# Kernel tuning notes

Measured on AMD Instinct MI355X. Metric: run time of the kernel, lower is better.

Reference implementation:

```python
import jax, jax.numpy as jnp
import numpy as np

V, D, H, L, DFF = 32000, 512, 8, 6, 2048
B, T = 64, 256
PAD_IDX = 1


def _pos_encoding(t, d):
    pos = jnp.arange(t, dtype=jnp.float32)[:, None]          # [t,1]
    i2 = jnp.arange(0, d, 2, dtype=jnp.float32)              # [d/2]
    ang = pos / jnp.power(10000.0, i2 / d)                   # [t,d/2]
    pe = jnp.zeros((t, d), dtype=jnp.float32)
    pe = pe.at[:, 0::2].set(jnp.sin(ang))
    pe = pe.at[:, 1::2].set(jnp.cos(ang))
    return pe


def _ln(x, g, b):
    mu = x.mean(-1, keepdims=True)
    var = ((x - mu) ** 2).mean(-1, keepdims=True)
    return (x - mu) * jax.lax.rsqrt(var + 1e-5) * g + b


def _mha(xq, xkv, Wq, Wk, Wv, Wo, bo, causal):
    b, tq, d = xq.shape
    tk = xkv.shape[1]
    hd = d // H
    q = (xq @ Wq).reshape(b, tq, H, hd)
    k = (xkv @ Wk).reshape(b, tk, H, hd)
    v = (xkv @ Wv).reshape(b, tk, H, hd)
    wei = jnp.einsum('bqhd,bkhd->bhqk', q, k) * (hd ** -0.5)
    if causal:
        mask = jnp.tril(jnp.ones((tq, tk), dtype=bool))
        wei = jnp.where(mask, wei, -jnp.inf)
    wei = jax.nn.softmax(wei, axis=-1)
    out = jnp.einsum('bhqk,bkhd->bqhd', wei, v).reshape(b, tq, d)
    return out @ Wo + bo


def _ffn(x, W1, b1, W2, b2):
    return jax.nn.relu(x @ W1 + b1) @ W2 + b2


def setup_inputs() -> dict:
    key = jax.random.key(0)
    ks = iter(jax.random.split(key, 64))
    nrm = lambda shape: (jax.random.normal(next(ks), shape, dtype=jnp.float32) * 0.02)
    inp = {
        'idx': jax.random.randint(next(ks), (B, T), 0, V),
        'idx_enc': jax.random.randint(next(ks), (B, T), 0, V),
        'targets': jax.random.randint(next(ks), (B, T), 0, V),
        'emb_dec': nrm((V, D)),
        'emb_enc': nrm((V, D)),
        # encoder stacks [L, ...]
        'enc_Wq': nrm((L, D, D)), 'enc_Wk': nrm((L, D, D)), 'enc_Wv': nrm((L, D, D)),
        'enc_Wo': nrm((L, D, D)), 'enc_bo': jnp.zeros((L, D)),
        'enc_ln_g': jnp.ones((L, 2, D)), 'enc_ln_b': jnp.zeros((L, 2, D)),
        'enc_W1': nrm((L, D, DFF)), 'enc_b1': jnp.zeros((L, DFF)),
        'enc_W2': nrm((L, DFF, D)), 'enc_b2': jnp.zeros((L, D)),
        # decoder stacks [L, ...]
        'dec_Wq_sa': nrm((L, D, D)), 'dec_Wk_sa': nrm((L, D, D)), 'dec_Wv_sa': nrm((L, D, D)),
        'dec_Wo_sa': nrm((L, D, D)), 'dec_bo_sa': jnp.zeros((L, D)),
        'dec_Wq_xa': nrm((L, D, D)), 'dec_Wk_xa': nrm((L, D, D)), 'dec_Wv_xa': nrm((L, D, D)),
        'dec_Wo_xa': nrm((L, D, D)), 'dec_bo_xa': jnp.zeros((L, D)),
        'dec_ln_g': jnp.ones((L, 4, D)), 'dec_ln_b': jnp.zeros((L, 4, D)),
        'dec_W1': nrm((L, D, DFF)), 'dec_b1': jnp.zeros((L, DFF)),
        'dec_W2': nrm((L, DFF, D)), 'dec_b2': jnp.zeros((L, D)),
        'lnf_g': jnp.ones((D,)), 'lnf_b': jnp.zeros((D,)),
        'Wlm': nrm((D, V)), 'blm': jnp.zeros((V,)),
    }
    return inp


def reference(idx, idx_enc, targets, emb_dec, emb_enc,
              enc_Wq, enc_Wk, enc_Wv, enc_Wo, enc_bo, enc_ln_g, enc_ln_b,
              enc_W1, enc_b1, enc_W2, enc_b2,
              dec_Wq_sa, dec_Wk_sa, dec_Wv_sa, dec_Wo_sa, dec_bo_sa,
              dec_Wq_xa, dec_Wk_xa, dec_Wv_xa, dec_Wo_xa, dec_bo_xa,
              dec_ln_g, dec_ln_b, dec_W1, dec_b1, dec_W2, dec_b2,
              lnf_g, lnf_b, Wlm, blm):
    t_dec = idx.shape[1]
    t_enc = idx_enc.shape[1]
    pe = _pos_encoding(256, D)
    # encoder
    y = emb_enc[idx_enc] + pe[:t_enc]
    for l in range(L):
        h = _ln(y, enc_ln_g[l, 0], enc_ln_b[l, 0])
        y = y + _mha(h, h, enc_Wq[l], enc_Wk[l], enc_Wv[l], enc_Wo[l], enc_bo[l], causal=False)
        h = _ln(y, enc_ln_g[l, 1], enc_ln_b[l, 1])
        y = y + _ffn(h, enc_W1[l], enc_b1[l], enc_W2[l], enc_b2[l])
    # decoder
    x = emb_dec[idx] + pe[:t_dec]
    for l in range(L):
        h = _ln(x, dec_ln_g[l, 0], dec_ln_b[l, 0])
        x = x + _mha(h, h, dec_Wq_sa[l], dec_Wk_sa[l], dec_Wv_sa[l], dec_Wo_sa[l], dec_bo_sa[l], causal=True)
        hq = _ln(x, dec_ln_g[l, 1], dec_ln_b[l, 1])
        hk = _ln(y, dec_ln_g[l, 2], dec_ln_b[l, 2])
        x = x + _mha(hq, hk, dec_Wq_xa[l], dec_Wk_xa[l], dec_Wv_xa[l], dec_Wo_xa[l], dec_bo_xa[l], causal=False)
        h = _ln(x, dec_ln_g[l, 3], dec_ln_b[l, 3])
        x = x + _ffn(h, dec_W1[l], dec_b1[l], dec_W2[l], dec_b2[l])
    x = _ln(x, lnf_g, lnf_b)
    logits = (x @ Wlm + blm).reshape(-1, V)  # [B*T, V]
    # cross entropy with ignore_index = PAD_IDX, mean over non-ignored
    tgt = targets.reshape(-1)
    logp = jax.nn.log_softmax(logits, axis=-1)
    nll = -jnp.take_along_axis(logp, tgt[:, None], axis=-1)[:, 0]
    valid = (tgt != PAD_IDX).astype(logits.dtype)
    loss = jnp.sum(nll * valid) / jnp.maximum(jnp.sum(valid), 1.0)
    return logits, loss
```

## Files before the change

kernel.cpp:

```cpp
#include <hip/hip_runtime.h>

typedef __attribute__((ext_vector_type(8))) short s8v;
typedef __attribute__((ext_vector_type(4))) float f4v;
using u16 = unsigned short;

__device__ __forceinline__ u16 f2bf(float f) {
  union { float f; unsigned u; } v; v.f = f;
  return (u16)((v.u + 0x7FFFu + ((v.u >> 16) & 1u)) >> 16);
}

__global__ __launch_bounds__(256) void pe_kernel(float* __restrict__ pe) {
  int i = blockIdx.x * 256 + threadIdx.x;
  int t = i >> 8, p = i & 255;
  float ex = (2.f * (float)p) / 512.f;
  float ang = (float)t * expf(-ex * 9.210340371976184f);
  pe[t * 512 + 2 * p]     = sinf(ang);
  pe[t * 512 + 2 * p + 1] = cosf(ang);
}

__global__ __launch_bounds__(256) void wconv_kernel(const float* __restrict__ in,
    u16* __restrict__ out, int R, int C, size_t dstride) {
  __shared__ float tile[64][65];
  const size_t mat = (size_t)R * C;
  const float* src = in + (size_t)blockIdx.z * mat;
  u16* dst = out + (size_t)blockIdx.z * dstride;
  int r0 = blockIdx.x * 64, c0 = blockIdx.y * 64;
  int tr = threadIdx.x >> 6, tc = threadIdx.x & 63;
#pragma unroll
  for (int i = 0; i < 16; ++i)
    tile[i * 4 + tr][tc] = src[(size_t)(r0 + i * 4 + tr) * C + (c0 + tc)];
  __syncthreads();
#pragma unroll
  for (int i = 0; i < 16; ++i)
    dst[(size_t)(c0 + i * 4 + tr) * R + (r0 + tc)] = f2bf(tile[tc][i * 4 + tr]);
}

__global__ __launch_bounds__(256) void embed_kernel(const int* __restrict__ idx,
    const float* __restrict__ emb, const float* __restrict__ pe, float* __restrict__ y) {
  int i = blockIdx.x * 256 + threadIdx.x;
  int row = i >> 7, c = (i & 127) * 4;
  int t = row & 255;
  int tok = idx[row];
  f4v e = *(const f4v*)(emb + (size_t)tok * 512 + c);
  f4v p = *(const f4v*)(pe + (size_t)t * 512 + c);
  *(f4v*)(y + (size_t)row * 512 + c) = e + p;
}

__global__ __launch_bounds__(256) void ln_kernel(const float* __restrict__ x,
    const float* __restrict__ g, const float* __restrict__ b, u16* __restrict__ out) {
  int row = blockIdx.x * 4 + (threadIdx.x >> 6);
  int lane = threadIdx.x & 63;
  const float* xr = x + (size_t)row * 512 + lane * 8;
  f4v v0 = *(const f4v*)xr;
  f4v v1 = *(const f4v*)(xr + 4);
  float s = v0[0] + v0[1] + v0[2] + v0[3] + v1[0] + v1[1] + v1[2] + v1[3];
#pragma unroll
  for (int o = 1; o < 64; o <<= 1) s += __shfl_xor(s, o);
  float mu = s * (1.f / 512.f);
  float q = 0.f;
#pragma unroll
  for (int j = 0; j < 4; ++j) {
    float d0 = v0[j] - mu; q += d0 * d0;
    float d1 = v1[j] - mu; q += d1 * d1;
  }
#pragma unroll
  for (int o = 1; o < 64; o <<= 1) q += __shfl_xor(q, o);
  float rs = rsqrtf(q * (1.f / 512.f) + 1e-5f);
  f4v g0 = *(const f4v*)(g + lane * 8), g1 = *(const f4v*)(g + lane * 8 + 4);
  f4v b0 = *(const f4v*)(b + lane * 8), b1 = *(const f4v*)(b + lane * 8 + 4);
  s8v ov;
#pragma unroll
  for (int j = 0; j < 4; ++j) {
    ov[j]     = (short)f2bf((v0[j] - mu) * rs * g0[j] + b0[j]);
    ov[4 + j] = (short)f2bf((v1[j] - mu) * rs * g1[j] + b1[j]);
  }
  *(s8v*)(out + (size_t)row * 512 + lane * 8) = ov;
}

template<int WR, int MW, int NW, int HAS_BIAS, int ADD_RES, int RELU,
         int OUT_BF16, int WLOSS, int NT>
__global__ __launch_bounds__(MW * NW * 64, 2) void gemm_mfma(
    const u16* __restrict__ A, const u16* __restrict__ Bt,
    const float* __restrict__ bias, const float* __restrict__ res,
    void* __restrict__ outp, int M, int N, int K,
    float* __restrict__ pmax, float* __restrict__ psum) {
  constexpr int BM = MW * WR * 16;
  constexpr int BN = NW * 64;
  constexpr int THREADS = MW * NW * 64;
  constexpr int STEP = THREADS / 8;
  __shared__ __align__(16) u16 As[2][BM * 64];
  __shared__ __align__(16) u16 Bs[2][BN * 64];
  const int tid = threadIdx.x, lane = tid & 63, w = tid >> 6;
  int nx = gridDim.x;
  int flat = blockIdx.y * nx + blockIdx.x;
  int per = (nx * gridDim.y) >> 3;
  int sw = (flat & 7) * per + (flat >> 3);
  int by = sw / nx, bx = sw - by * nx;
  const int m0 = bx * BM, n0 = by * BN;
  const int wm = (w / NW) * (WR * 16), wn = (w % NW) * 64;
  const int lhi = lane >> 4, llo = lane & 15;
  const int srow = tid >> 3;
  const int sl = tid & 7;
  const int gcol = (sl ^ (srow & 7)) * 8;

  const u16* Ag = A + (size_t)(m0 + srow) * K + gcol;
  const u16* Bg = Bt + (size_t)(n0 + srow) * K + gcol;
  const size_t rstep = (size_t)STEP * K;

  auto STAGE = [&](int b, int kt) {
#pragma unroll
    for (int q = 0; q < BM / STEP; ++q)
      __builtin_amdgcn_global_load_lds(
          (const __attribute__((address_space(1))) void*)(Ag + q * rstep + kt),
          (__attribute__((address_space(3))) void*)(&As[b][(q * STEP + srow) * 64 + sl * 8]),
          16, 0, 0);
#pragma unroll
    for (int q = 0; q < BN / STEP; ++q)
      __builtin_amdgcn_global_load_lds(
          (const __attribute__((address_space(1))) void*)(Bg + q * rstep + kt),
          (__attribute__((address_space(3))) void*)(&Bs[b][(q * STEP + srow) * 64 + sl * 8]),
          16, 0, 0);
  };
  const int sx = llo & 7;

  f4v acc[WR][4] = {};
  const int nk = K >> 6;
  STAGE(0, 0);
  asm volatile("s_waitcnt vmcnt(0)" ::: "memory");
  __builtin_amdgcn_s_barrier();
  __builtin_amdgcn_sched_barrier(0);
  int cur = 0;
  for (int t = 0; t < nk; ++t) {
    if (t + 1 < nk) STAGE(cur ^ 1, (t + 1) * 64);
#pragma unroll
    for (int kk = 0; kk < 2; ++kk) {
      s8v af[WR], bfv[4];
#pragma unroll
      for (int i = 0; i < WR; ++i)
        af[i] = *(const s8v*)&As[cur][(wm + i * 16 + llo) * 64 + (((kk * 4 + lhi) ^ sx) * 8)];
#pragma unroll
      for (int j = 0; j < 4; ++j)
        bfv[j] = *(const s8v*)&Bs[cur][(wn + j * 16 + llo) * 64 + (((kk * 4 + lhi) ^ sx) * 8)];
      __builtin_amdgcn_s_setprio(1);
#pragma unroll
      for (int i = 0; i < WR; ++i)
#pragma unroll
        for (int j = 0; j < 4; ++j)
          acc[i][j] = __builtin_amdgcn_mfma_f32_16x16x32_bf16(af[i], bfv[j], acc[i][j], 0, 0, 0);
      __builtin_amdgcn_s_setprio(0);
    }
    asm volatile("s_waitcnt vmcnt(0)" ::: "memory");
    __builtin_amdgcn_s_barrier();
    __builtin_amdgcn_sched_barrier(0);
    cur ^= 1;
  }

  if (OUT_BF16) {
    float bvj[4];
#pragma unroll
    for (int j = 0; j < 4; ++j)
      bvj[j] = HAS_BIAS ? bias[n0 + wn + j * 16 + llo] : 0.f;
#pragma unroll
    for (int i = 0; i < WR; ++i) {
#pragma unroll
      for (int j = 0; j < 4; ++j) {
        int col = n0 + wn + j * 16 + llo;
#pragma unroll
        for (int r = 0; r < 4; ++r) {
          int row = m0 + wm + i * 16 + lhi * 4 + r;
          float v = acc[i][j][r] + bvj[j];
          if (RELU) v = fmaxf(v, 0.f);
          ((u16*)outp)[(size_t)row * N + col] = f2bf(v);
        }
      }
    }
  } else {
    float* lb = (float*)&As[0][0];
    float* wbuf = lb + w * 1088;
    f4v bias4 = {0.f, 0.f, 0.f, 0.f};
    if (HAS_BIAS) bias4 = *(const f4v*)(bias + n0 + wn + llo * 4);
    float* lbm = lb + 9216;
    float* lbs = lb + 10240;
#pragma unroll
    for (int i = 0; i < WR; ++i) {
#pragma unroll
      for (int j = 0; j < 4; ++j)
#pragma unroll
        for (int r = 0; r < 4; ++r)
          wbuf[(lhi * 4 + r) * 68 + j * 16 + llo] = acc[i][j][r];
      asm volatile("s_waitcnt lgkmcnt(0)" ::: "memory");
      __builtin_amdgcn_sched_barrier(0);
#pragma unroll
      for (int p = 0; p < 4; ++p) {
        int r16 = p * 4 + lhi;
        f4v v4 = *(const f4v*)&wbuf[r16 * 68 + llo * 4];
        v4 += bias4;
        int grow = m0 + wm + i * 16 + r16;
        int gcol4 = n0 + wn + llo * 4;
        if (ADD_RES) v4 += *(const f4v*)(res + (size_t)grow * N + gcol4);
        if (RELU) {
          v4[0] = fmaxf(v4[0], 0.f); v4[1] = fmaxf(v4[1], 0.f);
          v4[2] = fmaxf(v4[2], 0.f); v4[3] = fmaxf(v4[3], 0.f);
        }
        float* dst = (float*)outp + (size_t)grow * N + gcol4;
        if (NT) __builtin_nontemporal_store(v4, (f4v*)dst);
        else    *(f4v*)dst = v4;
        if (WLOSS) {
          float mx = fmaxf(fmaxf(v4[0], v4[1]), fmaxf(v4[2], v4[3]));
          mx = fmaxf(mx, __shfl_xor(mx, 1));
          mx = fmaxf(mx, __shfl_xor(mx, 2));
          mx = fmaxf(mx, __shfl_xor(mx, 4));
          mx = fmaxf(mx, __shfl_xor(mx, 8));
          float sum = __expf(v4[0] - mx) + __expf(v4[1] - mx)
                    + __expf(v4[2] - mx) + __expf(v4[3] - mx);
          sum += __shfl_xor(sum, 1); sum += __shfl_xor(sum, 2);
          sum += __shfl_xor(sum, 4); sum += __shfl_xor(sum, 8);
          if (llo == 0) {
            int lr = wm + i * 16 + r16;
            lbm[lr * 4 + (wn >> 6)] = mx;
            lbs[lr * 4 + (wn >> 6)] = sum;
          }
        }
      }
      asm volatile("s_waitcnt lgkmcnt(0)" ::: "memory");
      __builtin_amdgcn_sched_barrier(0);
    }
    if (WLOSS) {
      __syncthreads();
      if (tid < 256) {
        float m = lbm[tid * 4];
        m = fmaxf(fmaxf(m, lbm[tid * 4 + 1]), fmaxf(lbm[tid * 4 + 2], lbm[tid * 4 + 3]));
        float ss = lbs[tid * 4 + 0] * __expf(lbm[tid * 4 + 0] - m)
                 + lbs[tid * 4 + 1] * __expf(lbm[tid * 4 + 1] - m)
                 + lbs[tid * 4 + 2] * __expf(lbm[tid * 4 + 2] - m)
                 + lbs[tid * 4 + 3] * __expf(lbm[tid * 4 + 3] - m);
        int ntile = N >> 8;
        pmax[(size_t)(m0 + tid) * ntile + by] = m;
        psum[(size_t)(m0 + tid) * ntile + by] = ss;
      }
    }
  }
}

__global__ __launch_bounds__(256) void attn_kernel(
    const u16* __restrict__ Qp, int qs, const u16* __restrict__ Kp,
    const u16* __restrict__ Vp, int kvs, u16* __restrict__ Ob, int causal) {
  __shared__ __align__(16) u16 Ks[256][72];
  __shared__ __align__(16) u16 Vt[64][264];
  __shared__ __align__(16) u16 Ps[4][16][264];
  const int tid = threadIdx.x, lane = tid & 63, w = tid >> 6;
  const int b = blockIdx.x >> 3, h = blockIdx.x & 7;
  const size_t qbase  = (size_t)b * 256 * qs  + (size_t)h * 64;
  const size_t kvbase = (size_t)b * 256 * kvs + (size_t)h * 64;
  const size_t obase  = (size_t)b * 256 * 512 + (size_t)h * 64;
  {
    int t0 = tid >> 3, d0 = (tid & 7) * 8;
#pragma unroll
    for (int it = 0; it < 8; ++it) {
      int t = it * 32 + t0;
      s8v kv = *(const s8v*)(Kp + kvbase + (size_t)t * kvs + d0);
      *(s8v*)&Ks[t][d0] = kv;
      s8v vv = *(const s8v*)(Vp + kvbase + (size_t)t * kvs + d0);
#pragma unroll
      for (int j = 0; j < 8; ++j) Vt[d0 + j][t] = (u16)vv[j];
    }
  }
  __syncthreads();
  const int lhi = lane >> 4, llo = lane & 15;
  for (int qc = 0; qc < 4; ++qc) {
    const int qr0 = w * 64 + qc * 16;
    s8v aq0 = *(const s8v*)(Qp + qbase + (size_t)(qr0 + llo) * qs + lhi * 8);
    s8v aq1 = *(const s8v*)(Qp + qbase + (size_t)(qr0 + llo) * qs + 32 + lhi * 8);
    f4v S[16];
#pragma unroll
    for (int c = 0; c < 16; ++c) {
      s8v bk0 = *(const s8v*)&Ks[c * 16 + llo][lhi * 8];
      s8v bk1 = *(const s8v*)&Ks[c * 16 + llo][32 + lhi * 8];
      f4v z = {0.f, 0.f, 0.f, 0.f};
      z = __builtin_amdgcn_mfma_f32_16x16x32_bf16(aq0, bk0, z, 0, 0, 0);
      S[c] = __builtin_amdgcn_mfma_f32_16x16x32_bf16(aq1, bk1, z, 0, 0, 0);
    }
#pragma unroll
    for (int r = 0; r < 4; ++r) {
      const int tq = qr0 + lhi * 4 + r;
      float mx = -1e30f;
#pragma unroll
      for (int c = 0; c < 16; ++c) {
        float s = S[c][r] * 0.125f;
        if (causal && (c * 16 + llo) > tq) s = -1e30f;
        S[c][r] = s;
        mx = fmaxf(mx, s);
      }
      mx = fmaxf(mx, __shfl_xor(mx, 1));
      mx = fmaxf(mx, __shfl_xor(mx, 2));
      mx = fmaxf(mx, __shfl_xor(mx, 4));
      mx = fmaxf(mx, __shfl_xor(mx, 8));
      float sum = 0.f;
#pragma unroll
      for (int c = 0; c < 16; ++c) { float p = __expf(S[c][r] - mx); S[c][r] = p; sum += p; }
      sum += __shfl_xor(sum, 1); sum += __shfl_xor(sum, 2);
      sum += __shfl_xor(sum, 4); sum += __shfl_xor(sum, 8);
      float inv = 1.f / sum;
#pragma unroll
      for (int c = 0; c < 16; ++c)
        Ps[w][lhi * 4 + r][c * 16 + llo] = f2bf(S[c][r] * inv);
    }
    asm volatile("s_waitcnt lgkmcnt(0)" ::: "memory");
    f4v o[4] = {};
#pragma unroll
    for (int kb = 0; kb < 8; ++kb) {
      s8v pa = *(const s8v*)&Ps[w][llo][kb * 32 + lhi * 8];
#pragma unroll
      for (int nb = 0; nb < 4; ++nb) {
        s8v bv = *(const s8v*)&Vt[nb * 16 + llo][kb * 32 + lhi * 8];
        o[nb] = __builtin_amdgcn_mfma_f32_16x16x32_bf16(pa, bv, o[nb], 0, 0, 0);
      }
    }
#pragma unroll
    for (int nb = 0; nb < 4; ++nb)
#pragma unroll
      for (int r = 0; r < 4; ++r)
        Ob[obase + (size_t)(qr0 + lhi * 4 + r) * 512 + nb * 16 + llo] = f2bf(o[nb][r]);
  }
}

__global__ __launch_bounds__(256) void loss_lse_kernel(const float* __restrict__ pmax,
    const float* __restrict__ psum, const float* __restrict__ logits,
    const int* __restrict__ tgt, float* __restrict__ nll, float* __restrict__ valid) {
  const int w = threadIdx.x >> 6, lane = threadIdx.x & 63;
  const int row = blockIdx.x * 4 + w;
  float m = -1e30f, s = 0.f;
  for (int e = lane; e < 125; e += 64) {
    float pm = pmax[(size_t)row * 125 + e], ps = psum[(size_t)row * 125 + e];
    if (pm > m) { s = s * __expf(m - pm) + ps; m = pm; }
    else          s += ps * __expf(pm - m);
  }
#pragma unroll
  for (int o = 1; o < 64; o <<= 1) {
    float om = __shfl_xor(m, o), os = __shfl_xor(s, o);
    float mm = fmaxf(m, om);
    s = s * __expf(m - mm) + os * __expf(om - mm);
    m = mm;
  }
  if (lane == 0) {
    int t = tgt[row];
    float lse = m + logf(s);
    float v = (t != 1) ? 1.f : 0.f;
    nll[row] = v * (lse - logits[(size_t)row * 32000 + t]);
    valid[row] = v;
  }
}

__global__ __launch_bounds__(256) void loss_final_kernel(const float* __restrict__ nll,
    const float* __restrict__ valid, float* __restrict__ out) {
  __shared__ float sa[256], sb[256];
  int tid = threadIdx.x;
  float s = 0.f, c = 0.f;
  for (int i = tid; i < 16384; i += 256) { s += nll[i]; c += valid[i]; }
  sa[tid] = s; sb[tid] = c;
  __syncthreads();
  for (int st = 128; st > 0; st >>= 1) {
    if (tid < st) { sa[tid] += sa[tid + st]; sb[tid] += sb[tid + st]; }
    __syncthreads();
  }
  if (tid == 0) out[0] = sa[0] / fmaxf(sb[0], 1.f);
}

extern "C" void kernel_launch(void* const* d_in, const int* in_sizes, int n_in,
                              void* d_out, int out_size, void* d_ws, size_t ws_size,
                              hipStream_t stream) {
  (void)in_sizes; (void)n_in; (void)out_size; (void)ws_size;
  const int* idx       = (const int*)d_in[0];
  const int* idx_enc   = (const int*)d_in[1];
  const int* targets   = (const int*)d_in[2];
  const float* emb_dec = (const float*)d_in[3];
  const float* emb_enc = (const float*)d_in[4];
  const float* enc_Wq  = (const float*)d_in[5];
  const float* enc_Wk  = (const float*)d_in[6];
  const float* enc_Wv  = (const float*)d_in[7];
  const float* enc_Wo  = (const float*)d_in[8];
  const float* enc_bo  = (const float*)d_in[9];
  const float* enc_ln_g = (const float*)d_in[10];
  const float* enc_ln_b = (const float*)d_in[11];
  const float* enc_W1  = (const float*)d_in[12];
  const float* enc_b1  = (const float*)d_in[13];
  const float* enc_W2  = (const float*)d_in[14];
  const float* enc_b2  = (const float*)d_in[15];
  const float* dWq_sa  = (const float*)d_in[16];
  const float* dWk_sa  = (const float*)d_in[17];
  const float* dWv_sa  = (const float*)d_in[18];
  const float* dWo_sa  = (const float*)d_in[19];
  const float* dbo_sa  = (const float*)d_in[20];
  const float* dWq_xa  = (const float*)d_in[21];
  const float* dWk_xa  = (const float*)d_in[22];
  const float* dWv_xa  = (const float*)d_in[23];
  const float* dWo_xa  = (const float*)d_in[24];
  const float* dbo_xa  = (const float*)d_in[25];
  const float* dec_ln_g = (const float*)d_in[26];
  const float* dec_ln_b = (const float*)d_in[27];
  const float* dec_W1  = (const float*)d_in[28];
  const float* dec_b1  = (const float*)d_in[29];
  const float* dec_W2  = (const float*)d_in[30];
  const float* dec_b2  = (const float*)d_in[31];
  const float* lnf_g   = (const float*)d_in[32];
  const float* lnf_b   = (const float*)d_in[33];
  const float* Wlm     = (const float*)d_in[34];
  const float* blm     = (const float*)d_in[35];
  float* out_logits = (float*)d_out;
  float* out_loss   = out_logits + (size_t)16384 * 32000;

  size_t off = 0;
  auto alloc = [&](size_t bytes) -> char* {
    char* p = (char*)d_ws + off;
    off += (bytes + 255) & ~(size_t)255;
    return p;
  };
  const size_t SQ = 512 * 512, SF = 512 * 2048;
  u16* tWqkvE = (u16*)alloc(6 * 3 * SQ * 2);
  u16* tWoE   = (u16*)alloc(6 * SQ * 2);
  u16* tW1E   = (u16*)alloc(6 * SF * 2);
  u16* tW2E   = (u16*)alloc(6 * SF * 2);
  u16* tWqkvS = (u16*)alloc(6 * 3 * SQ * 2);
  u16* tWoS   = (u16*)alloc(6 * SQ * 2);
  u16* tWqX   = (u16*)alloc(6 * SQ * 2);
  u16* tWkvX  = (u16*)alloc(6 * 2 * SQ * 2);
  u16* tWoX   = (u16*)alloc(6 * SQ * 2);
  u16* tW1D   = (u16*)alloc(6 * SF * 2);
  u16* tW2D   = (u16*)alloc(6 * SF * 2);
  u16* tWlm   = (u16*)alloc((size_t)32000 * 512 * 2);
  float* pe   = (float*)alloc(256 * 512 * 4);
  float* yE   = (float*)alloc((size_t)16384 * 512 * 4);
  float* xD   = (float*)alloc((size_t)16384 * 512 * 4);
  u16* hA     = (u16*)alloc((size_t)16384 * 512 * 2);
  u16* hB     = (u16*)alloc((size_t)16384 * 512 * 2);
  u16* qkvB   = (u16*)alloc((size_t)16384 * 1536 * 2);
  u16* qB     = (u16*)alloc((size_t)16384 * 512 * 2);
  u16* kvB    = (u16*)alloc((size_t)16384 * 1024 * 2);
  u16* atB    = (u16*)alloc((size_t)16384 * 512 * 2);
  u16* midB   = (u16*)alloc((size_t)16384 * 2048 * 2);
  float* pmax = (float*)alloc((size_t)16384 * 125 * 4);
  float* psum = (float*)alloc((size_t)16384 * 125 * 4);
  float* rnll = (float*)alloc(16384 * 4);
  float* rval = (float*)alloc(16384 * 4);

  dim3 tb(256);
  const size_t S3 = 3 * SQ, S2 = 2 * SQ;
  wconv_kernel<<<dim3(8, 8, 6), tb, 0, stream>>>(enc_Wq, tWqkvE + 0 * SQ, 512, 512, S3);
  wconv_kernel<<<dim3(8, 8, 6), tb, 0, stream>>>(enc_Wk, tWqkvE + 1 * SQ, 512, 512, S3);
  wconv_kernel<<<dim3(8, 8, 6), tb, 0, stream>>>(enc_Wv, tWqkvE + 2 * SQ, 512, 512, S3);
  wconv_kernel<<<dim3(8, 8, 6), tb, 0, stream>>>(enc_Wo, tWoE, 512, 512, SQ);
  wconv_kernel<<<dim3(8, 32, 6), tb, 0, stream>>>(enc_W1, tW1E, 512, 2048, SF);
  wconv_kernel<<<dim3(32, 8, 6), tb, 0, stream>>>(enc_W2, tW2E, 2048, 512, SF);
  wconv_kernel<<<dim3(8, 8, 6), tb, 0, stream>>>(dWq_sa, tWqkvS + 0 * SQ, 512, 512, S3);
  wconv_kernel<<<dim3(8, 8, 6), tb, 0, stream>>>(dWk_sa, tWqkvS + 1 * SQ, 512, 512, S3);
  wconv_kernel<<<dim3(8, 8, 6), tb, 0, stream>>>(dWv_sa, tWqkvS + 2 * SQ, 512, 512, S3);
  wconv_kernel<<<dim3(8, 8, 6), tb, 0, stream>>>(dWo_sa, tWoS, 512, 512, SQ);
  wconv_kernel<<<dim3(8, 8, 6), tb, 0, stream>>>(dWq_xa, tWqX, 512, 512, SQ);
  wconv_kernel<<<dim3(8, 8, 6), tb, 0, stream>>>(dWk_xa, tWkvX + 0 * SQ, 512, 512, S2);
  wconv_kernel<<<dim3(8, 8, 6), tb, 0, stream>>>(dWv_xa, tWkvX + 1 * SQ, 512, 512, S2);
  wconv_kernel<<<dim3(8, 8, 6), tb, 0, stream>>>(dWo_xa, tWoX, 512, 512, SQ);
  wconv_kernel<<<dim3(8, 32, 6), tb, 0, stream>>>(dec_W1, tW1D, 512, 2048, SF);
  wconv_kernel<<<dim3(32, 8, 6), tb, 0, stream>>>(dec_W2, tW2D, 2048, 512, SF);
  wconv_kernel<<<dim3(8, 500, 1), tb, 0, stream>>>(Wlm, tWlm, 512, 32000, (size_t)0);
  pe_kernel<<<256, 256, 0, stream>>>(pe);

  auto ln = [&](const float* xin, const float* g, const float* bb, u16* o) {
    ln_kernel<<<4096, 256, 0, stream>>>(xin, g, bb, o);
  };
  auto g_bf16_sm = [&](const u16* Ap, const u16* Bp, u16* Op, int N) {
    gemm_mfma<4, 2, 2, 0, 0, 0, 1, 0, 0><<<dim3(128, N / 128), 256, 0, stream>>>(
        Ap, Bp, nullptr, nullptr, Op, 16384, N, 512, nullptr, nullptr);
  };
  auto proj_res = [&](const u16* Ap, const u16* Bp, const float* bi, float* xr, int K) {
    gemm_mfma<4, 2, 2, 1, 1, 0, 0, 0, 0><<<dim3(128, 4), 256, 0, stream>>>(
        Ap, Bp, bi, xr, xr, 16384, 512, K, nullptr, nullptr);
  };
  auto ffn1 = [&](const u16* Ap, const u16* Bp, const float* bi, u16* Op) {
    gemm_mfma<8, 2, 4, 1, 0, 1, 1, 0, 0><<<dim3(64, 8), 512, 0, stream>>>(
        Ap, Bp, bi, nullptr, Op, 16384, 2048, 512, nullptr, nullptr);
  };

  embed_kernel<<<8192, 256, 0, stream>>>(idx_enc, emb_enc, pe, yE);
  for (int l = 0; l < 6; ++l) {
    ln(yE, enc_ln_g + (l * 2 + 0) * 512, enc_ln_b + (l * 2 + 0) * 512, hA);
    g_bf16_sm(hA, tWqkvE + l * S3, qkvB, 1536);
    attn_kernel<<<512, 256, 0, stream>>>(qkvB, 1536, qkvB + 512, qkvB + 1024, 1536, atB, 0);
    proj_res(atB, tWoE + l * SQ, enc_bo + l * 512, yE, 512);
    ln(yE, enc_ln_g + (l * 2 + 1) * 512, enc_ln_b + (l * 2 + 1) * 512, hA);
    ffn1(hA, tW1E + l * SF, enc_b1 + l * 2048, midB);
    proj_res(midB, tW2E + l * SF, enc_b2 + l * 512, yE, 2048);
  }

  embed_kernel<<<8192, 256, 0, stream>>>(idx, emb_dec, pe, xD);
  for (int l = 0; l < 6; ++l) {
    ln(xD, dec_ln_g + (l * 4 + 0) * 512, dec_ln_b + (l * 4 + 0) * 512, hA);
    g_bf16_sm(hA, tWqkvS + l * S3, qkvB, 1536);
    attn_kernel<<<512, 256, 0, stream>>>(qkvB, 1536, qkvB + 512, qkvB + 1024, 1536, atB, 1);
    proj_res(atB, tWoS + l * SQ, dbo_sa + l * 512, xD, 512);
    ln(xD, dec_ln_g + (l * 4 + 1) * 512, dec_ln_b + (l * 4 + 1) * 512, hA);
    ln(yE, dec_ln_g + (l * 4 + 2) * 512, dec_ln_b + (l * 4 + 2) * 512, hB);
    g_bf16_sm(hA, tWqX + l * SQ, qB, 512);
    g_bf16_sm(hB, tWkvX + l * S2, kvB, 1024);
    attn_kernel<<<512, 256, 0, stream>>>(qB, 512, kvB, kvB + 512, 1024, atB, 0);
    proj_res(atB, tWoX + l * SQ, dbo_xa + l * 512, xD, 512);
    ln(xD, dec_ln_g + (l * 4 + 3) * 512, dec_ln_b + (l * 4 + 3) * 512, hA);
    ffn1(hA, tW1D + l * SF, dec_b1 + l * 2048, midB);
    proj_res(midB, tW2D + l * SF, dec_b2 + l * 512, xD, 2048);
  }

  ln(xD, lnf_g, lnf_b, hA);
  gemm_mfma<8, 2, 4, 1, 0, 0, 0, 1, 1><<<dim3(64, 125), 512, 0, stream>>>(
      hA, tWlm, blm, nullptr, out_logits, 16384, 32000, 512, pmax, psum);
  loss_lse_kernel<<<4096, 256, 0, stream>>>(pmax, psum, out_logits, targets, rnll, rval);
  loss_final_kernel<<<1, 256, 0, stream>>>(rnll, rval, out_loss);
}
```

Baseline: 5.159 ms.

## Replace GEMM with triple-buffered 256x128 tile kernel for all projections

Replaces the templated double-buffered MFMA GEMM with a single 512-thread kernel that uses a fixed 256x128 tile and a three-stage LDS ring, prefetching two K-steps ahead with partial vmcnt waits. All projection, FFN and LM-head GEMMs now share this tile shape, which changes the grids and doubles the number of per-row partial max/sum tiles for the loss. The aim is to hide global-to-LDS latency better and to standardise tile reuse. In exchange it uses more LDS, allows only one block per CU, and the larger M tile reduces the number of blocks for the N=512 GEMMs.

```diff
diff --git a/kernel.cpp b/kernel.cpp
--- a/kernel.cpp
+++ b/kernel.cpp
@@ -77,27 +77,22 @@
   *(s8v*)(out + (size_t)row * 512 + lane * 8) = ov;
 }
 
-template<int WR, int MW, int NW, int HAS_BIAS, int ADD_RES, int RELU,
-         int OUT_BF16, int WLOSS, int NT>
-__global__ __launch_bounds__(MW * NW * 64, 2) void gemm_mfma(
+template<int HAS_BIAS, int ADD_RES, int RELU, int OUT_BF16, int WLOSS, int NT>
+__global__ __launch_bounds__(512, 1) void gemm3r(
     const u16* __restrict__ A, const u16* __restrict__ Bt,
     const float* __restrict__ bias, const float* __restrict__ res,
     void* __restrict__ outp, int M, int N, int K,
     float* __restrict__ pmax, float* __restrict__ psum) {
-  constexpr int BM = MW * WR * 16;
-  constexpr int BN = NW * 64;
-  constexpr int THREADS = MW * NW * 64;
-  constexpr int STEP = THREADS / 8;
-  __shared__ __align__(16) u16 As[2][BM * 64];
-  __shared__ __align__(16) u16 Bs[2][BN * 64];
+  __shared__ __align__(16) u16 As[3][256 * 64];
+  __shared__ __align__(16) u16 Bs[3][128 * 64];
   const int tid = threadIdx.x, lane = tid & 63, w = tid >> 6;
   int nx = gridDim.x;
   int flat = blockIdx.y * nx + blockIdx.x;
   int per = (nx * gridDim.y) >> 3;
   int sw = (flat & 7) * per + (flat >> 3);
   int by = sw / nx, bx = sw - by * nx;
-  const int m0 = bx * BM, n0 = by * BN;
-  const int wm = (w / NW) * (WR * 16), wn = (w % NW) * 64;
+  const int m0 = bx * 256, n0 = by * 128;
+  const int wm = (w >> 1) * 64, wn = (w & 1) * 64;
   const int lhi = lane >> 4, llo = lane & 15;
   const int srow = tid >> 3;
   const int sl = tid & 7;
@@ -105,54 +100,57 @@
 
   const u16* Ag = A + (size_t)(m0 + srow) * K + gcol;
   const u16* Bg = Bt + (size_t)(n0 + srow) * K + gcol;
-  const size_t rstep = (size_t)STEP * K;
+  const size_t rstep = (size_t)64 * K;
 
   auto STAGE = [&](int b, int kt) {
 #pragma unroll
-    for (int q = 0; q < BM / STEP; ++q)
+    for (int q = 0; q < 4; ++q)
       __builtin_amdgcn_global_load_lds(
           (const __attribute__((address_space(1))) void*)(Ag + q * rstep + kt),
-          (__attribute__((address_space(3))) void*)(&As[b][(q * STEP + srow) * 64 + sl * 8]),
+          (__attribute__((address_space(3))) void*)(&As[b][(q * 64 + srow) * 64 + sl * 8]),
           16, 0, 0);
 #pragma unroll
-    for (int q = 0; q < BN / STEP; ++q)
+    for (int q = 0; q < 2; ++q)
       __builtin_amdgcn_global_load_lds(
           (const __attribute__((address_space(1))) void*)(Bg + q * rstep + kt),
-          (__attribute__((address_space(3))) void*)(&Bs[b][(q * STEP + srow) * 64 + sl * 8]),
+          (__attribute__((address_space(3))) void*)(&Bs[b][(q * 64 + srow) * 64 + sl * 8]),
           16, 0, 0);
   };
   const int sx = llo & 7;
 
-  f4v acc[WR][4] = {};
+  f4v acc[4][4] = {};
   const int nk = K >> 6;
   STAGE(0, 0);
-  asm volatile("s_waitcnt vmcnt(0)" ::: "memory");
+  STAGE(1, 64);
+  asm volatile("s_waitcnt vmcnt(6)" ::: "memory");
   __builtin_amdgcn_s_barrier();
   __builtin_amdgcn_sched_barrier(0);
-  int cur = 0;
+  int cur = 0, nxt = 2;
   for (int t = 0; t < nk; ++t) {
-    if (t + 1 < nk) STAGE(cur ^ 1, (t + 1) * 64);
+    if (t + 2 < nk) STAGE(nxt, (t + 2) * 64);
 #pragma unroll
     for (int kk = 0; kk < 2; ++kk) {
-      s8v af[WR], bfv[4];
-#pragma unroll
-      for (int i = 0; i < WR; ++i)
+      s8v af[4], bfv[4];
+#pragma unroll
+      for (int i = 0; i < 4; ++i)
         af[i] = *(const s8v*)&As[cur][(wm + i * 16 + llo) * 64 + (((kk * 4 + lhi) ^ sx) * 8)];
 #pragma unroll
       for (int j = 0; j < 4; ++j)
         bfv[j] = *(const s8v*)&Bs[cur][(wn + j * 16 + llo) * 64 + (((kk * 4 + lhi) ^ sx) * 8)];
       __builtin_amdgcn_s_setprio(1);
 #pragma unroll
-      for (int i = 0; i < WR; ++i)
+      for (int i = 0; i < 4; ++i)
 #pragma unroll
         for (int j = 0; j < 4; ++j)
           acc[i][j] = __builtin_amdgcn_mfma_f32_16x16x32_bf16(af[i], bfv[j], acc[i][j], 0, 0, 0);
       __builtin_amdgcn_s_setprio(0);
     }
-    asm volatile("s_waitcnt vmcnt(0)" ::: "memory");
+    if (t + 2 < nk) asm volatile("s_waitcnt vmcnt(6)" ::: "memory");
+    else            asm volatile("s_waitcnt vmcnt(0)" ::: "memory");
     __builtin_amdgcn_s_barrier();
     __builtin_amdgcn_sched_barrier(0);
-    cur ^= 1;
+    cur = (cur == 2) ? 0 : cur + 1;
+    nxt = (nxt == 2) ? 0 : nxt + 1;
   }
 
   if (OUT_BF16) {
@@ -161,7 +159,7 @@
     for (int j = 0; j < 4; ++j)
       bvj[j] = HAS_BIAS ? bias[n0 + wn + j * 16 + llo] : 0.f;
 #pragma unroll
-    for (int i = 0; i < WR; ++i) {
+    for (int i = 0; i < 4; ++i) {
 #pragma unroll
       for (int j = 0; j < 4; ++j) {
         int col = n0 + wn + j * 16 + llo;
@@ -175,14 +173,13 @@
       }
     }
   } else {
-    float* lb = (float*)&As[0][0];
-    float* wbuf = lb + w * 1088;
+    float* wbuf = (float*)&As[0][0] + w * 1088;
+    float* lbm = (float*)&Bs[0][0];
+    float* lbs = lbm + 512;
     f4v bias4 = {0.f, 0.f, 0.f, 0.f};
     if (HAS_BIAS) bias4 = *(const f4v*)(bias + n0 + wn + llo * 4);
-    float* lbm = lb + 9216;
-    float* lbs = lb + 10240;
-#pragma unroll
-    for (int i = 0; i < WR; ++i) {
+#pragma unroll
+    for (int i = 0; i < 4; ++i) {
 #pragma unroll
       for (int j = 0; j < 4; ++j)
 #pragma unroll
@@ -217,8 +214,8 @@
           sum += __shfl_xor(sum, 4); sum += __shfl_xor(sum, 8);
           if (llo == 0) {
             int lr = wm + i * 16 + r16;
-            lbm[lr * 4 + (wn >> 6)] = mx;
-            lbs[lr * 4 + (wn >> 6)] = sum;
+            lbm[lr * 2 + (wn >> 6)] = mx;
+            lbs[lr * 2 + (wn >> 6)] = sum;
           }
         }
       }
@@ -228,13 +225,11 @@
     if (WLOSS) {
       __syncthreads();
       if (tid < 256) {
-        float m = lbm[tid * 4];
-        m = fmaxf(fmaxf(m, lbm[tid * 4 + 1]), fmaxf(lbm[tid * 4 + 2], lbm[tid * 4 + 3]));
-        float ss = lbs[tid * 4 + 0] * __expf(lbm[tid * 4 + 0] - m)
-                 + lbs[tid * 4 + 1] * __expf(lbm[tid * 4 + 1] - m)
-                 + lbs[tid * 4 + 2] * __expf(lbm[tid * 4 + 2] - m)
-                 + lbs[tid * 4 + 3] * __expf(lbm[tid * 4 + 3] - m);
-        int ntile = N >> 8;
+        float ma = lbm[tid * 2], mb = lbm[tid * 2 + 1];
+        float sa = lbs[tid * 2], sb = lbs[tid * 2 + 1];
+        float m = fmaxf(ma, mb);
+        float ss = sa * __expf(ma - m) + sb * __expf(mb - m);
+        int ntile = N >> 7;
         pmax[(size_t)(m0 + tid) * ntile + by] = m;
         psum[(size_t)(m0 + tid) * ntile + by] = ss;
       }
@@ -330,8 +325,8 @@
   const int w = threadIdx.x >> 6, lane = threadIdx.x & 63;
   const int row = blockIdx.x * 4 + w;
   float m = -1e30f, s = 0.f;
-  for (int e = lane; e < 125; e += 64) {
-    float pm = pmax[(size_t)row * 125 + e], ps = psum[(size_t)row * 125 + e];
+  for (int e = lane; e < 250; e += 64) {
+    float pm = pmax[(size_t)row * 250 + e], ps = psum[(size_t)row * 250 + e];
     if (pm > m) { s = s * __expf(m - pm) + ps; m = pm; }
     else          s += ps * __expf(pm - m);
   }
@@ -438,8 +433,8 @@
   u16* kvB    = (u16*)alloc((size_t)16384 * 1024 * 2);
   u16* atB    = (u16*)alloc((size_t)16384 * 512 * 2);
   u16* midB   = (u16*)alloc((size_t)16384 * 2048 * 2);
-  float* pmax = (float*)alloc((size_t)16384 * 125 * 4);
-  float* psum = (float*)alloc((size_t)16384 * 125 * 4);
+  float* pmax = (float*)alloc((size_t)16384 * 250 * 4);
+  float* psum = (float*)alloc((size_t)16384 * 250 * 4);
   float* rnll = (float*)alloc(16384 * 4);
   float* rval = (float*)alloc(16384 * 4);
 
@@ -467,23 +462,23 @@
   auto ln = [&](const float* xin, const float* g, const float* bb, u16* o) {
     ln_kernel<<<4096, 256, 0, stream>>>(xin, g, bb, o);
   };
-  auto g_bf16_sm = [&](const u16* Ap, const u16* Bp, u16* Op, int N) {
-    gemm_mfma<4, 2, 2, 0, 0, 0, 1, 0, 0><<<dim3(128, N / 128), 256, 0, stream>>>(
+  auto g_bf16 = [&](const u16* Ap, const u16* Bp, u16* Op, int N) {
+    gemm3r<0, 0, 0, 1, 0, 0><<<dim3(64, N / 128), 512, 0, stream>>>(
         Ap, Bp, nullptr, nullptr, Op, 16384, N, 512, nullptr, nullptr);
   };
   auto proj_res = [&](const u16* Ap, const u16* Bp, const float* bi, float* xr, int K) {
-    gemm_mfma<4, 2, 2, 1, 1, 0, 0, 0, 0><<<dim3(128, 4), 256, 0, stream>>>(
+    gemm3r<1, 1, 0, 0, 0, 0><<<dim3(64, 4), 512, 0, stream>>>(
         Ap, Bp, bi, xr, xr, 16384, 512, K, nullptr, nullptr);
   };
   auto ffn1 = [&](const u16* Ap, const u16* Bp, const float* bi, u16* Op) {
-    gemm_mfma<8, 2, 4, 1, 0, 1, 1, 0, 0><<<dim3(64, 8), 512, 0, stream>>>(
+    gemm3r<1, 0, 1, 1, 0, 0><<<dim3(64, 16), 512, 0, stream>>>(
         Ap, Bp, bi, nullptr, Op, 16384, 2048, 512, nullptr, nullptr);
   };
 
   embed_kernel<<<8192, 256, 0, stream>>>(idx_enc, emb_enc, pe, yE);
   for (int l = 0; l < 6; ++l) {
     ln(yE, enc_ln_g + (l * 2 + 0) * 512, enc_ln_b + (l * 2 + 0) * 512, hA);
-    g_bf16_sm(hA, tWqkvE + l * S3, qkvB, 1536);
+    g_bf16(hA, tWqkvE + l * S3, qkvB, 1536);
     attn_kernel<<<512, 256, 0, stream>>>(qkvB, 1536, qkvB + 512, qkvB + 1024, 1536, atB, 0);
     proj_res(atB, tWoE + l * SQ, enc_bo + l * 512, yE, 512);
     ln(yE, enc_ln_g + (l * 2 + 1) * 512, enc_ln_b + (l * 2 + 1) * 512, hA);
@@ -494,13 +489,13 @@
   embed_kernel<<<8192, 256, 0, stream>>>(idx, emb_dec, pe, xD);
   for (int l = 0; l < 6; ++l) {
     ln(xD, dec_ln_g + (l * 4 + 0) * 512, dec_ln_b + (l * 4 + 0) * 512, hA);
-    g_bf16_sm(hA, tWqkvS + l * S3, qkvB, 1536);
+    g_bf16(hA, tWqkvS + l * S3, qkvB, 1536);
     attn_kernel<<<512, 256, 0, stream>>>(qkvB, 1536, qkvB + 512, qkvB + 1024, 1536, atB, 1);
     proj_res(atB, tWoS + l * SQ, dbo_sa + l * 512, xD, 512);
     ln(xD, dec_ln_g + (l * 4 + 1) * 512, dec_ln_b + (l * 4 + 1) * 512, hA);
     ln(yE, dec_ln_g + (l * 4 + 2) * 512, dec_ln_b + (l * 4 + 2) * 512, hB);
-    g_bf16_sm(hA, tWqX + l * SQ, qB, 512);
-    g_bf16_sm(hB, tWkvX + l * S2, kvB, 1024);
+    g_bf16(hA, tWqX + l * SQ, qB, 512);
+    g_bf16(hB, tWkvX + l * S2, kvB, 1024);
     attn_kernel<<<512, 256, 0, stream>>>(qB, 512, kvB, kvB + 512, 1024, atB, 0);
     proj_res(atB, tWoX + l * SQ, dbo_xa + l * 512, xD, 512);
     ln(xD, dec_ln_g + (l * 4 + 3) * 512, dec_ln_b + (l * 4 + 3) * 512, hA);
@@ -509,7 +504,7 @@
   }
 
   ln(xD, lnf_g, lnf_b, hA);
-  gemm_mfma<8, 2, 4, 1, 0, 0, 0, 1, 1><<<dim3(64, 125), 512, 0, stream>>>(
+  gemm3r<1, 0, 0, 0, 1, 1><<<dim3(64, 250), 512, 0, stream>>>(
       hA, tWlm, blm, nullptr, out_logits, 16384, 32000, 512, pmax, psum);
   loss_lse_kernel<<<4096, 256, 0, stream>>>(pmax, psum, out_logits, targets, rnll, rval);
   loss_final_kernel<<<1, 256, 0, stream>>>(rnll, rval, out_loss);
```

Result: slower. 6.023 ms (+16.8%).
